# Performance work log

Hardware: AMD Instinct MI355X
Metric: run time of the kernel (lower is better)

Reference implementation:

```python
import jax, jax.numpy as jnp
import numpy as np

H, D_MODEL, LEN_Q, LEN_K, D_K, D_V = 16, 1024, 512, 2048, 64, 64
B = 4

def setup_inputs() -> dict:
    key = jax.random.key(0)
    ks = jax.random.split(key, 16)
    s = 0.02
    return {
        "Q": jax.random.normal(ks[0], (B, LEN_Q, D_MODEL), jnp.float32),
        "K": jax.random.normal(ks[1], (B, LEN_K, D_MODEL), jnp.float32),
        "V": jax.random.normal(ks[2], (B, LEN_K, D_MODEL), jnp.float32),
        "node_num": LEN_Q,
        "mask": jax.random.randint(ks[3], (B, LEN_K), 0, 2, jnp.int32),
        # params (stored as [in, out] so y = x @ W + b)
        "Wq": jax.random.normal(ks[4], (D_MODEL, H * D_K), jnp.float32) * s,
        "bq": jnp.zeros((H * D_K,), jnp.float32),
        "Wk": jax.random.normal(ks[5], (D_MODEL, H * D_K), jnp.float32) * s,
        "bk": jnp.zeros((H * D_K,), jnp.float32),
        "Wv": jax.random.normal(ks[6], (D_MODEL, H * D_V), jnp.float32) * s,
        "bv": jnp.zeros((H * D_V,), jnp.float32),
        "Wo": jax.random.normal(ks[7], (H * D_V, D_MODEL), jnp.float32) * s,
        "bo": jnp.zeros((D_MODEL,), jnp.float32),
        "gamma": jnp.ones((D_MODEL,), jnp.float32),
        "beta": jnp.zeros((D_MODEL,), jnp.float32),
    }

def _layernorm(x, gamma, beta, eps=1e-5):
    mu = jnp.mean(x, axis=-1, keepdims=True)
    var = jnp.mean((x - mu) ** 2, axis=-1, keepdims=True)
    return (x - mu) * jax.lax.rsqrt(var + eps) * gamma + beta

def reference(Q, K, V, node_num, mask, Wq, bq, Wk, bk, Wv, bv, Wo, bo, gamma, beta):
    b, lq, _ = Q.shape
    lk = K.shape[1]
    q = (Q @ Wq + bq).reshape(b, lq, H, D_K)   # [B, Lq, h, dk]
    k = (K @ Wk + bk).reshape(b, lk, H, D_K)   # [B, Lk, h, dk]
    v = (V @ Wv + bv).reshape(b, lk, H, D_V)   # [B, Lk, h, dv]
    scores = jnp.einsum('bqhd,bkhd->bhqk', q, k) / jnp.sqrt(jnp.float32(D_K))
    scores = jnp.where(mask[:, None, None, :] == 0, -jnp.inf, scores)
    alpha = jax.nn.softmax(scores, axis=-1)    # [B, h, Lq, Lk]
    out = jnp.einsum('bhqk,bkhd->bqhd', alpha, v).reshape(b, lq, H * D_V)
    out = out @ Wo + bo + Q                    # dropout is identity (eval)
    return _layernorm(out, gamma, beta)
```

## Files before the change

### kernel.cpp

```cpp
#include <hip/hip_runtime.h>

typedef __attribute__((ext_vector_type(8))) __bf16 bf16x8;
typedef __attribute__((ext_vector_type(4))) float f32x4;
typedef __attribute__((ext_vector_type(8))) unsigned short u16x8;

__device__ __forceinline__ float bf2f(unsigned short h) {
  union { unsigned int u; float f; } a; a.u = ((unsigned int)h) << 16; return a.f;
}
__device__ __forceinline__ unsigned short f2bf(float f) {
  union { float f; unsigned int u; } a; a.f = f;
  unsigned int u = a.u;
  u += 0x7fffu + ((u >> 16) & 1u);
  return (unsigned short)(u >> 16);
}
__device__ __forceinline__ float fast_exp2(float x) {
#if __has_builtin(__builtin_amdgcn_exp2f)
  return __builtin_amdgcn_exp2f(x);
#else
  return exp2f(x);
#endif
}
__device__ __forceinline__ bf16x8 ld_frag(const unsigned short* p) {
  bf16x8 r; __builtin_memcpy(&r, p, 16); return r;
}
__device__ __forceinline__ void cp16(unsigned short* dst, const unsigned short* src) {
  u16x8 t; __builtin_memcpy(&t, src, 16); __builtin_memcpy(dst, &t, 16);
}

#if __has_builtin(__builtin_amdgcn_global_load_lds)
typedef __attribute__((address_space(3))) unsigned int lds_u32;
typedef const __attribute__((address_space(1))) unsigned int glb_u32;
__device__ __forceinline__ void gload16(const unsigned short* g, unsigned short* l) {
  __builtin_amdgcn_global_load_lds((glb_u32*)g, (lds_u32*)l, 16, 0, 0);
}
#else
__device__ __forceinline__ void gload16(const unsigned short* g, unsigned short* l) {
  cp16(l, g);
}
#endif

__global__ __launch_bounds__(256) void cvt_kernel(
    const float* __restrict__ in, unsigned short* __restrict__ out, int n8)
{
  int i = blockIdx.x * 256 + threadIdx.x;
  if (i >= n8) return;
  float tf[8]; __builtin_memcpy(tf, &in[(size_t)i * 8], 32);
  unsigned short tu[8];
#pragma unroll
  for (int j = 0; j < 8; j++) tu[j] = f2bf(tf[j]);
  __builtin_memcpy(&out[(size_t)i * 8], tu, 16);
}

__global__ __launch_bounds__(256) void transpose4_kernel(
    const float* __restrict__ w0, const float* __restrict__ w1,
    const float* __restrict__ w2, const float* __restrict__ w3,
    unsigned short* __restrict__ out)
{
  __shared__ unsigned short tile[64 * 65];
  const int z = blockIdx.z;
  const float* in = (z == 0) ? w0 : (z == 1) ? w1 : (z == 2) ? w2 : w3;
  unsigned short* o = out + (size_t)z * 1048576;
  const int dim = 1024;
  const int t = threadIdx.x;
  const int n0 = blockIdx.x * 64, k0 = blockIdx.y * 64;
#pragma unroll
  for (int e = 0; e < 16; e++) {
    int idx = e * 256 + t;
    int i = idx >> 6, j = idx & 63;
    tile[i * 65 + j] = f2bf(in[(size_t)(k0 + i) * dim + n0 + j]);
  }
  __syncthreads();
#pragma unroll
  for (int e = 0; e < 16; e++) {
    int idx = e * 256 + t;
    int i = idx >> 6, j = idx & 63;
    o[(size_t)(n0 + i) * dim + k0 + j] = tile[j * 65 + i];
  }
}

__global__ __launch_bounds__(256) void gemm_bt_kernel(
    const unsigned short* __restrict__ A,
    const unsigned short* __restrict__ BT,
    const float* __restrict__ bias,
    unsigned short* __restrict__ C,
    int M, int N, int K, float cscale)
{
  __shared__ unsigned short As[128 * 32];
  __shared__ unsigned short Bs[128 * 32];
  const int tid  = threadIdx.x;
  const int wave = tid >> 6;
  const int lane = tid & 63;
  const int quad = lane >> 4;
  const int l16  = lane & 15;
  const int m0 = blockIdx.x * 128;
  const int n0 = blockIdx.y * 128;
  const int wm = (wave & 1) * 64;
  const int wn = (wave >> 1) * 64;

  const f32x4 fz = {0.0f, 0.0f, 0.0f, 0.0f};
  f32x4 acc[4][4];
#pragma unroll
  for (int i = 0; i < 4; i++)
#pragma unroll
    for (int j = 0; j < 4; j++) acc[i][j] = fz;

  const int srow0 = tid >> 2;
  const int scol  = (tid & 3) * 8;

  for (int k0 = 0; k0 < K; k0 += 32) {
#pragma unroll
    for (int i = 0; i < 2; i++) {
      int row = srow0 + i * 64;
      gload16(&A[(size_t)(m0 + row) * K + k0 + scol], &As[row * 32 + scol]);
      gload16(&BT[(size_t)(n0 + row) * K + k0 + scol], &Bs[row * 32 + scol]);
    }
    __syncthreads();
    bf16x8 afr[4], bfr[4];
#pragma unroll
    for (int mt = 0; mt < 4; mt++) afr[mt] = ld_frag(&As[(wm + mt * 16 + l16) * 32 + quad * 8]);
#pragma unroll
    for (int nt = 0; nt < 4; nt++) bfr[nt] = ld_frag(&Bs[(wn + nt * 16 + l16) * 32 + quad * 8]);
#pragma unroll
    for (int mt = 0; mt < 4; mt++)
#pragma unroll
      for (int nt = 0; nt < 4; nt++)
        acc[mt][nt] = __builtin_amdgcn_mfma_f32_16x16x32_bf16(afr[mt], bfr[nt], acc[mt][nt], 0, 0, 0);
    __syncthreads();
  }

#pragma unroll
  for (int nt = 0; nt < 4; nt++) {
    int col = n0 + wn + nt * 16 + l16;
    float bv = bias[col];
#pragma unroll
    for (int mt = 0; mt < 4; mt++) {
      int rowb = m0 + wm + mt * 16 + quad * 4;
#pragma unroll
      for (int r = 0; r < 4; r++)
        C[(size_t)(rowb + r) * N + col] = f2bf((acc[mt][nt][r] + bv) * cscale);
    }
  }
}

__global__ __launch_bounds__(256) void gemm_bt64_kernel(
    const unsigned short* __restrict__ A,
    const unsigned short* __restrict__ BT,
    const float* __restrict__ bias,
    unsigned short* __restrict__ C,
    int M, int N, int K, float cscale)
{
  __shared__ unsigned short As[64 * 32];
  __shared__ unsigned short Bs[128 * 32];
  const int tid  = threadIdx.x;
  const int wave = tid >> 6;
  const int lane = tid & 63;
  const int quad = lane >> 4;
  const int l16  = lane & 15;
  const int m0 = blockIdx.x * 64;
  const int n0 = blockIdx.y * 128;
  const int wm = (wave & 1) * 32;
  const int wn = (wave >> 1) * 64;

  const f32x4 fz = {0.0f, 0.0f, 0.0f, 0.0f};
  f32x4 acc[2][4];
#pragma unroll
  for (int i = 0; i < 2; i++)
#pragma unroll
    for (int j = 0; j < 4; j++) acc[i][j] = fz;

  const int srow0 = tid >> 2;
  const int scol  = (tid & 3) * 8;

  for (int k0 = 0; k0 < K; k0 += 32) {
    gload16(&A[(size_t)(m0 + srow0) * K + k0 + scol], &As[srow0 * 32 + scol]);
#pragma unroll
    for (int i = 0; i < 2; i++) {
      int row = srow0 + i * 64;
      gload16(&BT[(size_t)(n0 + row) * K + k0 + scol], &Bs[row * 32 + scol]);
    }
    __syncthreads();
    bf16x8 afr[2], bfr[4];
#pragma unroll
    for (int mt = 0; mt < 2; mt++) afr[mt] = ld_frag(&As[(wm + mt * 16 + l16) * 32 + quad * 8]);
#pragma unroll
    for (int nt = 0; nt < 4; nt++) bfr[nt] = ld_frag(&Bs[(wn + nt * 16 + l16) * 32 + quad * 8]);
#pragma unroll
    for (int mt = 0; mt < 2; mt++)
#pragma unroll
      for (int nt = 0; nt < 4; nt++)
        acc[mt][nt] = __builtin_amdgcn_mfma_f32_16x16x32_bf16(afr[mt], bfr[nt], acc[mt][nt], 0, 0, 0);
    __syncthreads();
  }

#pragma unroll
  for (int nt = 0; nt < 4; nt++) {
    int col = n0 + wn + nt * 16 + l16;
    float bv = bias[col];
#pragma unroll
    for (int mt = 0; mt < 2; mt++) {
      int rowb = m0 + wm + mt * 16 + quad * 4;
#pragma unroll
      for (int r = 0; r < 4; r++)
        C[(size_t)(rowb + r) * N + col] = f2bf((acc[mt][nt][r] + bv) * cscale);
    }
  }
}

__global__ __launch_bounds__(256) void gemm_vt_kernel(
    const unsigned short* __restrict__ A,
    const unsigned short* __restrict__ BT,
    const float* __restrict__ bias,
    unsigned short* __restrict__ vt)
{
  __shared__ unsigned short As[128 * 32];
  __shared__ unsigned short Bs[128 * 32];
  __shared__ unsigned short Ts[4][64 * 72];
  const int K = 1024;
  const int tid  = threadIdx.x;
  const int wave = tid >> 6;
  const int lane = tid & 63;
  const int quad = lane >> 4;
  const int l16  = lane & 15;
  const int m0 = blockIdx.x * 128;
  const int n0 = blockIdx.y * 128;
  const int wm = (wave & 1) * 64;
  const int wn = (wave >> 1) * 64;

  const f32x4 fz = {0.0f, 0.0f, 0.0f, 0.0f};
  f32x4 acc[4][4];
#pragma unroll
  for (int i = 0; i < 4; i++)
#pragma unroll
    for (int j = 0; j < 4; j++) acc[i][j] = fz;

  const int srow0 = tid >> 2;
  const int scol  = (tid & 3) * 8;

  for (int k0 = 0; k0 < K; k0 += 32) {
#pragma unroll
    for (int i = 0; i < 2; i++) {
      int row = srow0 + i * 64;
      gload16(&A[(size_t)(m0 + row) * K + k0 + scol], &As[row * 32 + scol]);
      gload16(&BT[(size_t)(n0 + row) * K + k0 + scol], &Bs[row * 32 + scol]);
    }
    __syncthreads();
    bf16x8 afr[4], bfr[4];
#pragma unroll
    for (int mt = 0; mt < 4; mt++) afr[mt] = ld_frag(&As[(wm + mt * 16 + l16) * 32 + quad * 8]);
#pragma unroll
    for (int nt = 0; nt < 4; nt++) bfr[nt] = ld_frag(&Bs[(wn + nt * 16 + l16) * 32 + quad * 8]);
#pragma unroll
    for (int mt = 0; mt < 4; mt++)
#pragma unroll
      for (int nt = 0; nt < 4; nt++)
        acc[mt][nt] = __builtin_amdgcn_mfma_f32_16x16x32_bf16(afr[mt], bfr[nt], acc[mt][nt], 0, 0, 0);
    __syncthreads();
  }

#pragma unroll
  for (int nt = 0; nt < 4; nt++) {
    float bv = bias[n0 + wn + nt * 16 + l16];
#pragma unroll
    for (int mt = 0; mt < 4; mt++)
#pragma unroll
      for (int r = 0; r < 4; r++)
        Ts[wave][(nt * 16 + l16) * 72 + mt * 16 + quad * 4 + r] = f2bf(acc[mt][nt][r] + bv);
  }
  {
    const int R0 = m0 + wm;
    const int b  = R0 >> 11;
    const int key0 = R0 & 2047;
    const int col = n0 + wn + lane;
    const int h  = col >> 6, dv = col & 63;
    const size_t vtrow = ((size_t)(b * 16 + h)) * 64 + dv;
#pragma unroll
    for (int jb = 0; jb < 8; jb++)
      cp16((unsigned short*)&vt[vtrow * 2048 + key0 + jb * 8],
           &Ts[wave][lane * 72 + jb * 8]);
  }
}

__device__ __forceinline__ void attn_load_tile(
    const unsigned short* __restrict__ kp, const unsigned short* __restrict__ vt,
    const int* __restrict__ mask, size_t kbase, size_t vbase, int mbase,
    int kt, int quad, int l16,
    bf16x8 (&bk)[4][2], bf16x8 (&bv)[4][2], int (&mk)[4])
{
#pragma unroll
  for (int nt = 0; nt < 4; nt++) {
    const size_t krow = kbase + ((size_t)(kt * 64 + nt * 16 + l16)) * 1024;
#pragma unroll
    for (int kc = 0; kc < 2; kc++)
      bk[nt][kc] = ld_frag(&kp[krow + kc * 32 + quad * 8]);
    mk[nt] = mask[mbase + kt * 64 + nt * 16 + l16];
  }
#pragma unroll
  for (int dvt = 0; dvt < 4; dvt++) {
    const size_t vrow = vbase + ((size_t)(dvt * 16 + l16)) * 2048 + kt * 64;
#pragma unroll
    for (int kc = 0; kc < 2; kc++)
      bv[dvt][kc] = ld_frag(&vt[vrow + kc * 32 + quad * 8]);
  }
}

__device__ __forceinline__ void attn_compute_tile(
    const bf16x8 (&aq)[2], const bf16x8 (&bk)[4][2], const bf16x8 (&bv)[4][2],
    const int (&mk)[4], unsigned short* Ps, int quad, int l16,
    float (&l_i)[4], f32x4 (&O)[4])
{
  const f32x4 fz = {0.0f, 0.0f, 0.0f, 0.0f};
  f32x4 s[4];
#pragma unroll
  for (int nt = 0; nt < 4; nt++) s[nt] = fz;
  __builtin_amdgcn_s_setprio(1);
#pragma unroll
  for (int nt = 0; nt < 4; nt++)
#pragma unroll
    for (int kc = 0; kc < 2; kc++)
      s[nt] = __builtin_amdgcn_mfma_f32_16x16x32_bf16(aq[kc], bk[nt][kc], s[nt], 0, 0, 0);
  __builtin_amdgcn_s_setprio(0);

#pragma unroll
  for (int nt = 0; nt < 4; nt++) {
    bool ok = (mk[nt] != 0);
#pragma unroll
    for (int r = 0; r < 4; r++) {
      float p = ok ? fast_exp2(s[nt][r]) : 0.0f;
      l_i[r] += p;
      Ps[(quad * 4 + r) * 72 + nt * 16 + l16] = f2bf(p);
    }
  }

  bf16x8 ap[2];
#pragma unroll
  for (int kc = 0; kc < 2; kc++)
    ap[kc] = ld_frag(&Ps[l16 * 72 + kc * 32 + quad * 8]);
  __builtin_amdgcn_s_setprio(1);
#pragma unroll
  for (int dvt = 0; dvt < 4; dvt++)
#pragma unroll
    for (int kc = 0; kc < 2; kc++)
      O[dvt] = __builtin_amdgcn_mfma_f32_16x16x32_bf16(ap[kc], bv[dvt][kc], O[dvt], 0, 0, 0);
  __builtin_amdgcn_s_setprio(0);
}

__global__ __launch_bounds__(256) void attn_kernel(
    const unsigned short* __restrict__ qp,
    const unsigned short* __restrict__ kp,
    const unsigned short* __restrict__ vt,
    const int* __restrict__ mask,
    unsigned short* __restrict__ attn)
{
  __shared__ unsigned short Ps[4][16 * 72];
  __shared__ unsigned short Opart[2][4][16 * 64];
  __shared__ float Lpart[2][4][16];

  const int tid  = threadIdx.x;
  const int wave = tid >> 6;
  const int lane = tid & 63;
  const int quad = lane >> 4;
  const int l16  = lane & 15;
  const int bid  = blockIdx.x;
  const int bh = bid & 63;
  const int qg = bid >> 6;
  const int b = bh >> 4, h = bh & 15;

  bf16x8 aq[2][2];
#pragma unroll
  for (int s = 0; s < 2; s++) {
    const size_t qbase = ((size_t)(b * 512 + qg * 32 + s * 16 + l16)) * 1024 + h * 64;
#pragma unroll
    for (int kc = 0; kc < 2; kc++)
      aq[s][kc] = ld_frag(&qp[qbase + kc * 32 + quad * 8]);
  }

  const f32x4 fz = {0.0f, 0.0f, 0.0f, 0.0f};
  float l_i[2][4];
  f32x4 O[2][4];
#pragma unroll
  for (int s = 0; s < 2; s++)
#pragma unroll
    for (int r = 0; r < 4; r++) { l_i[s][r] = 0.0f; O[s][r] = fz; }

  const size_t kbase = ((size_t)(b * 2048)) * 1024 + h * 64;
  const size_t vbase = ((size_t)(bh * 64)) * 2048;
  const int mbase = b * 2048;

  for (int it = 0; it < 8; it++) {
    const int kt = it * 4 + wave;
    bf16x8 bk[4][2], bv[4][2]; int mk[4];
    attn_load_tile(kp, vt, mask, kbase, vbase, mbase, kt, quad, l16, bk, bv, mk);
    attn_compute_tile(aq[0], bk, bv, mk, Ps[wave], quad, l16, l_i[0], O[0]);
    attn_compute_tile(aq[1], bk, bv, mk, Ps[wave], quad, l16, l_i[1], O[1]);
  }

#pragma unroll
  for (int s = 0; s < 2; s++)
#pragma unroll
    for (int off = 1; off < 16; off <<= 1)
#pragma unroll
      for (int r = 0; r < 4; r++) l_i[s][r] += __shfl_xor(l_i[s][r], off);

#pragma unroll
  for (int s = 0; s < 2; s++) {
#pragma unroll
    for (int dvt = 0; dvt < 4; dvt++)
#pragma unroll
      for (int r = 0; r < 4; r++)
        Opart[s][wave][(quad * 4 + r) * 64 + dvt * 16 + l16] = f2bf(O[s][dvt][r]);
    if (l16 == 0) {
#pragma unroll
      for (int r = 0; r < 4; r++)
        Lpart[s][wave][quad * 4 + r] = l_i[s][r];
    }
  }
  __syncthreads();

#pragma unroll
  for (int s = 0; s < 2; s++) {
#pragma unroll
    for (int r = 0; r < 4; r++) {
      const int row = quad * 4 + r;
      float lsum = Lpart[s][0][row] + Lpart[s][1][row] + Lpart[s][2][row] + Lpart[s][3][row];
      float inv = (lsum > 0.0f) ? (1.0f / lsum) : 0.0f;
      float of = 0.0f;
#pragma unroll
      for (int w = 0; w < 4; w++)
        of += bf2f(Opart[s][w][row * 64 + wave * 16 + l16]);
      const int grow = b * 512 + qg * 32 + s * 16 + row;
      attn[(size_t)grow * 1024 + h * 64 + wave * 16 + l16] = f2bf(of * inv);
    }
  }
}

__global__ __launch_bounds__(256) void ln_kernel(
    const unsigned short* __restrict__ x,
    const float* __restrict__ resid,
    const float* __restrict__ gamma,
    const float* __restrict__ beta,
    float* __restrict__ out)
{
  const int row = blockIdx.x;
  const int t = threadIdx.x;
  const int wave = t >> 6, lane = t & 63;
  __shared__ float red[8];
  float v[4];
  float s1 = 0.0f, s2 = 0.0f;
#pragma unroll
  for (int i = 0; i < 4; i++) {
    int e = t + i * 256;
    float val = bf2f(x[(size_t)row * 1024 + e]) + resid[(size_t)row * 1024 + e];
    v[i] = val; s1 += val; s2 += val * val;
  }
#pragma unroll
  for (int off = 1; off < 64; off <<= 1) { s1 += __shfl_xor(s1, off); s2 += __shfl_xor(s2, off); }
  if (lane == 0) { red[wave] = s1; red[4 + wave] = s2; }
  __syncthreads();
  s1 = red[0] + red[1] + red[2] + red[3];
  s2 = red[4] + red[5] + red[6] + red[7];
  float mu  = s1 * (1.0f / 1024.0f);
  float var = s2 * (1.0f / 1024.0f) - mu * mu;
  float rstd = rsqrtf(var + 1e-5f);
#pragma unroll
  for (int i = 0; i < 4; i++) {
    int e = t + i * 256;
    out[(size_t)row * 1024 + e] = (v[i] - mu) * rstd * gamma[e] + beta[e];
  }
}

extern "C" void kernel_launch(void* const* d_in, const int* in_sizes, int n_in,
                              void* d_out, int out_size, void* d_ws, size_t ws_size,
                              hipStream_t stream) {
  (void)out_size; (void)ws_size;
  const float* Q = (const float*)d_in[0];
  const float* K = (const float*)d_in[1];
  const float* V = (const float*)d_in[2];

  int ix = 3;
  if (ix < n_in && in_sizes[ix] == 1) ix++;
  const int* mask  = (const int*)d_in[ix++];
  const float* Wq = (const float*)d_in[ix++]; const float* bq = (const float*)d_in[ix++];
  const float* Wk = (const float*)d_in[ix++]; const float* bk = (const float*)d_in[ix++];
  const float* Wv = (const float*)d_in[ix++]; const float* bv = (const float*)d_in[ix++];
  const float* Wo = (const float*)d_in[ix++]; const float* bo = (const float*)d_in[ix++];
  const float* gm = (const float*)d_in[ix++]; const float* bt = (const float*)d_in[ix++];

  char* ws = (char*)d_ws;
  dim3 blk(256);

  unsigned short* WT4 = (unsigned short*)(ws);
  unsigned short* qp  = (unsigned short*)(ws + (8ull  << 20));
  unsigned short* kp  = (unsigned short*)(ws + (12ull << 20));
  unsigned short* vt  = (unsigned short*)(ws + (28ull << 20));
  unsigned short* at  = (unsigned short*)(ws + (44ull << 20));
  unsigned short* qb  = at;
  unsigned short* kvb = (unsigned short*)(ws + (48ull << 20));

  cvt_kernel<<<dim3(1024), blk, 0, stream>>>(Q, qb, 262144);
  cvt_kernel<<<dim3(4096), blk, 0, stream>>>(K, kvb, 1048576);
  transpose4_kernel<<<dim3(16, 16, 4), blk, 0, stream>>>(Wq, Wk, Wv, Wo, WT4);

  gemm_bt64_kernel<<<dim3(32, 8), blk, 0, stream>>>(qb, WT4, bq, qp, 2048, 1024, 1024, 0.18033688011112042f);
  gemm_bt_kernel<<<dim3(64, 8), blk, 0, stream>>>(kvb, WT4 + 1048576, bk, kp, 8192, 1024, 1024, 1.0f);
  cvt_kernel<<<dim3(4096), blk, 0, stream>>>(V, kvb, 1048576);
  gemm_vt_kernel<<<dim3(64, 8), blk, 0, stream>>>(kvb, WT4 + 2097152, bv, vt);

  attn_kernel<<<dim3(1024), blk, 0, stream>>>(qp, kp, vt, mask, at);

  gemm_bt64_kernel<<<dim3(32, 8), blk, 0, stream>>>(at, WT4 + 3145728, bo, qp, 2048, 1024, 1024, 1.0f);
  ln_kernel<<<dim3(2048), blk, 0, stream>>>(qp, Q, gm, bt, (float*)d_out);
}
```

Measured before the change: 317.8 us.

## Double-buffer GEMM LDS tiles and split attention blocks into 16-row query groups

All three projection GEMM kernels now use two LDS buffers. The next K-slice is issued before computing the current one, with explicit vmcnt waits and raw s_barrier calls in place of __syncthreads, so global loads overlap with MFMA work. The attention kernel now handles 16 query rows per block instead of 32 and launches twice as many blocks. This raises parallelism and cuts register and LDS use, but each K/V tile is loaded from memory twice as often. The hand-coded vmcnt counts assume gload16 is tracked by the vector-memory counter, so the prefetch is only correct if that holds.

Measured after the change: 366.9 us. 1.15x slower.

```diff
diff --git a/kernel.cpp b/kernel.cpp
--- a/kernel.cpp
+++ b/kernel.cpp
@@ -85,8 +85,8 @@
     unsigned short* __restrict__ C,
     int M, int N, int K, float cscale)
 {
-  __shared__ unsigned short As[128 * 32];
-  __shared__ unsigned short Bs[128 * 32];
+  __shared__ unsigned short As[2][128 * 32];
+  __shared__ unsigned short Bs[2][128 * 32];
   const int tid  = threadIdx.x;
   const int wave = tid >> 6;
   const int lane = tid & 63;
@@ -105,27 +105,38 @@
     for (int j = 0; j < 4; j++) acc[i][j] = fz;
 
   const int srow0 = tid >> 2;
+  const int srow1 = srow0 + 64;
   const int scol  = (tid & 3) * 8;
 
-  for (int k0 = 0; k0 < K; k0 += 32) {
-#pragma unroll
-    for (int i = 0; i < 2; i++) {
-      int row = srow0 + i * 64;
-      gload16(&A[(size_t)(m0 + row) * K + k0 + scol], &As[row * 32 + scol]);
-      gload16(&BT[(size_t)(n0 + row) * K + k0 + scol], &Bs[row * 32 + scol]);
+  auto stage = [&](int bf, int k0) {
+    gload16(&A[(size_t)(m0 + srow0) * K + k0 + scol], &As[bf][srow0 * 32 + scol]);
+    gload16(&A[(size_t)(m0 + srow1) * K + k0 + scol], &As[bf][srow1 * 32 + scol]);
+    gload16(&BT[(size_t)(n0 + srow0) * K + k0 + scol], &Bs[bf][srow0 * 32 + scol]);
+    gload16(&BT[(size_t)(n0 + srow1) * K + k0 + scol], &Bs[bf][srow1 * 32 + scol]);
+  };
+
+  const int NT = K >> 5;
+  stage(0, 0);
+  for (int kt = 0; kt < NT; ++kt) {
+    const int cur = kt & 1;
+    if (kt + 1 < NT) {
+      stage(cur ^ 1, (kt + 1) << 5);
+      asm volatile("s_waitcnt vmcnt(4)" ::: "memory");
+    } else {
+      asm volatile("s_waitcnt vmcnt(0)" ::: "memory");
     }
-    __syncthreads();
+    __builtin_amdgcn_s_barrier();
     bf16x8 afr[4], bfr[4];
 #pragma unroll
-    for (int mt = 0; mt < 4; mt++) afr[mt] = ld_frag(&As[(wm + mt * 16 + l16) * 32 + quad * 8]);
-#pragma unroll
-    for (int nt = 0; nt < 4; nt++) bfr[nt] = ld_frag(&Bs[(wn + nt * 16 + l16) * 32 + quad * 8]);
+    for (int mt = 0; mt < 4; mt++) afr[mt] = ld_frag(&As[cur][(wm + mt * 16 + l16) * 32 + quad * 8]);
+#pragma unroll
+    for (int nt = 0; nt < 4; nt++) bfr[nt] = ld_frag(&Bs[cur][(wn + nt * 16 + l16) * 32 + quad * 8]);
 #pragma unroll
     for (int mt = 0; mt < 4; mt++)
 #pragma unroll
       for (int nt = 0; nt < 4; nt++)
         acc[mt][nt] = __builtin_amdgcn_mfma_f32_16x16x32_bf16(afr[mt], bfr[nt], acc[mt][nt], 0, 0, 0);
-    __syncthreads();
+    __builtin_amdgcn_s_barrier();
   }
 
 #pragma unroll
@@ -149,8 +160,8 @@
     unsigned short* __restrict__ C,
     int M, int N, int K, float cscale)
 {
-  __shared__ unsigned short As[64 * 32];
-  __shared__ unsigned short Bs[128 * 32];
+  __shared__ unsigned short As[2][64 * 32];
+  __shared__ unsigned short Bs[2][128 * 32];
   const int tid  = threadIdx.x;
   const int wave = tid >> 6;
   const int lane = tid & 63;
@@ -169,27 +180,37 @@
     for (int j = 0; j < 4; j++) acc[i][j] = fz;
 
   const int srow0 = tid >> 2;
+  const int srow1 = srow0 + 64;
   const int scol  = (tid & 3) * 8;
 
-  for (int k0 = 0; k0 < K; k0 += 32) {
-    gload16(&A[(size_t)(m0 + srow0) * K + k0 + scol], &As[srow0 * 32 + scol]);
-#pragma unroll
-    for (int i = 0; i < 2; i++) {
-      int row = srow0 + i * 64;
-      gload16(&BT[(size_t)(n0 + row) * K + k0 + scol], &Bs[row * 32 + scol]);
+  auto stage = [&](int bf, int k0) {
+    gload16(&A[(size_t)(m0 + srow0) * K + k0 + scol], &As[bf][srow0 * 32 + scol]);
+    gload16(&BT[(size_t)(n0 + srow0) * K + k0 + scol], &Bs[bf][srow0 * 32 + scol]);
+    gload16(&BT[(size_t)(n0 + srow1) * K + k0 + scol], &Bs[bf][srow1 * 32 + scol]);
+  };
+
+  const int NT = K >> 5;
+  stage(0, 0);
+  for (int kt = 0; kt < NT; ++kt) {
+    const int cur = kt & 1;
+    if (kt + 1 < NT) {
+      stage(cur ^ 1, (kt + 1) << 5);
+      asm volatile("s_waitcnt vmcnt(3)" ::: "memory");
+    } else {
+      asm volatile("s_waitcnt vmcnt(0)" ::: "memory");
     }
-    __syncthreads();
+    __builtin_amdgcn_s_barrier();
     bf16x8 afr[2], bfr[4];
 #pragma unroll
-    for (int mt = 0; mt < 2; mt++) afr[mt] = ld_frag(&As[(wm + mt * 16 + l16) * 32 + quad * 8]);
-#pragma unroll
-    for (int nt = 0; nt < 4; nt++) bfr[nt] = ld_frag(&Bs[(wn + nt * 16 + l16) * 32 + quad * 8]);
+    for (int mt = 0; mt < 2; mt++) afr[mt] = ld_frag(&As[cur][(wm + mt * 16 + l16) * 32 + quad * 8]);
+#pragma unroll
+    for (int nt = 0; nt < 4; nt++) bfr[nt] = ld_frag(&Bs[cur][(wn + nt * 16 + l16) * 32 + quad * 8]);
 #pragma unroll
     for (int mt = 0; mt < 2; mt++)
 #pragma unroll
       for (int nt = 0; nt < 4; nt++)
         acc[mt][nt] = __builtin_amdgcn_mfma_f32_16x16x32_bf16(afr[mt], bfr[nt], acc[mt][nt], 0, 0, 0);
-    __syncthreads();
+    __builtin_amdgcn_s_barrier();
   }
 
 #pragma unroll
@@ -212,8 +233,8 @@
     const float* __restrict__ bias,
     unsigned short* __restrict__ vt)
 {
-  __shared__ unsigned short As[128 * 32];
-  __shared__ unsigned short Bs[128 * 32];
+  __shared__ unsigned short As[2][128 * 32];
+  __shared__ unsigned short Bs[2][128 * 32];
   __shared__ unsigned short Ts[4][64 * 72];
   const int K = 1024;
   const int tid  = threadIdx.x;
@@ -234,27 +255,38 @@
     for (int j = 0; j < 4; j++) acc[i][j] = fz;
 
   const int srow0 = tid >> 2;
+  const int srow1 = srow0 + 64;
   const int scol  = (tid & 3) * 8;
 
-  for (int k0 = 0; k0 < K; k0 += 32) {
-#pragma unroll
-    for (int i = 0; i < 2; i++) {
-      int row = srow0 + i * 64;
-      gload16(&A[(size_t)(m0 + row) * K + k0 + scol], &As[row * 32 + scol]);
-      gload16(&BT[(size_t)(n0 + row) * K + k0 + scol], &Bs[row * 32 + scol]);
+  auto stage = [&](int bf, int k0) {
+    gload16(&A[(size_t)(m0 + srow0) * K + k0 + scol], &As[bf][srow0 * 32 + scol]);
+    gload16(&A[(size_t)(m0 + srow1) * K + k0 + scol], &As[bf][srow1 * 32 + scol]);
+    gload16(&BT[(size_t)(n0 + srow0) * K + k0 + scol], &Bs[bf][srow0 * 32 + scol]);
+    gload16(&BT[(size_t)(n0 + srow1) * K + k0 + scol], &Bs[bf][srow1 * 32 + scol]);
+  };
+
+  const int NT = K >> 5;
+  stage(0, 0);
+  for (int kt = 0; kt < NT; ++kt) {
+    const int cur = kt & 1;
+    if (kt + 1 < NT) {
+      stage(cur ^ 1, (kt + 1) << 5);
+      asm volatile("s_waitcnt vmcnt(4)" ::: "memory");
+    } else {
+      asm volatile("s_waitcnt vmcnt(0)" ::: "memory");
     }
-    __syncthreads();
+    __builtin_amdgcn_s_barrier();
     bf16x8 afr[4], bfr[4];
 #pragma unroll
-    for (int mt = 0; mt < 4; mt++) afr[mt] = ld_frag(&As[(wm + mt * 16 + l16) * 32 + quad * 8]);
-#pragma unroll
-    for (int nt = 0; nt < 4; nt++) bfr[nt] = ld_frag(&Bs[(wn + nt * 16 + l16) * 32 + quad * 8]);
+    for (int mt = 0; mt < 4; mt++) afr[mt] = ld_frag(&As[cur][(wm + mt * 16 + l16) * 32 + quad * 8]);
+#pragma unroll
+    for (int nt = 0; nt < 4; nt++) bfr[nt] = ld_frag(&Bs[cur][(wn + nt * 16 + l16) * 32 + quad * 8]);
 #pragma unroll
     for (int mt = 0; mt < 4; mt++)
 #pragma unroll
       for (int nt = 0; nt < 4; nt++)
         acc[mt][nt] = __builtin_amdgcn_mfma_f32_16x16x32_bf16(afr[mt], bfr[nt], acc[mt][nt], 0, 0, 0);
-    __syncthreads();
+    __builtin_amdgcn_s_barrier();
   }
 
 #pragma unroll
@@ -352,8 +384,8 @@
     unsigned short* __restrict__ attn)
 {
   __shared__ unsigned short Ps[4][16 * 72];
-  __shared__ unsigned short Opart[2][4][16 * 64];
-  __shared__ float Lpart[2][4][16];
+  __shared__ unsigned short Opart[4][16 * 64];
+  __shared__ float Lpart[4][16];
 
   const int tid  = threadIdx.x;
   const int wave = tid >> 6;
@@ -365,22 +397,19 @@
   const int qg = bid >> 6;
   const int b = bh >> 4, h = bh & 15;
 
-  bf16x8 aq[2][2];
-#pragma unroll
-  for (int s = 0; s < 2; s++) {
-    const size_t qbase = ((size_t)(b * 512 + qg * 32 + s * 16 + l16)) * 1024 + h * 64;
+  bf16x8 aq[2];
+  {
+    const size_t qbase = ((size_t)(b * 512 + qg * 16 + l16)) * 1024 + h * 64;
 #pragma unroll
     for (int kc = 0; kc < 2; kc++)
-      aq[s][kc] = ld_frag(&qp[qbase + kc * 32 + quad * 8]);
+      aq[kc] = ld_frag(&qp[qbase + kc * 32 + quad * 8]);
   }
 
   const f32x4 fz = {0.0f, 0.0f, 0.0f, 0.0f};
-  float l_i[2][4];
-  f32x4 O[2][4];
-#pragma unroll
-  for (int s = 0; s < 2; s++)
-#pragma unroll
-    for (int r = 0; r < 4; r++) { l_i[s][r] = 0.0f; O[s][r] = fz; }
+  float l_i[4];
+  f32x4 O[4];
+#pragma unroll
+  for (int r = 0; r < 4; r++) { l_i[r] = 0.0f; O[r] = fz; }
 
   const size_t kbase = ((size_t)(b * 2048)) * 1024 + h * 64;
   const size_t vbase = ((size_t)(bh * 64)) * 2048;
@@ -390,46 +419,37 @@
     const int kt = it * 4 + wave;
     bf16x8 bk[4][2], bv[4][2]; int mk[4];
     attn_load_tile(kp, vt, mask, kbase, vbase, mbase, kt, quad, l16, bk, bv, mk);
-    attn_compute_tile(aq[0], bk, bv, mk, Ps[wave], quad, l16, l_i[0], O[0]);
-    attn_compute_tile(aq[1], bk, bv, mk, Ps[wave], quad, l16, l_i[1], O[1]);
-  }
-
-#pragma unroll
-  for (int s = 0; s < 2; s++)
-#pragma unroll
-    for (int off = 1; off < 16; off <<= 1)
-#pragma unroll
-      for (int r = 0; r < 4; r++) l_i[s][r] += __shfl_xor(l_i[s][r], off);
-
-#pragma unroll
-  for (int s = 0; s < 2; s++) {
-#pragma unroll
-    for (int dvt = 0; dvt < 4; dvt++)
-#pragma unroll
-      for (int r = 0; r < 4; r++)
-        Opart[s][wave][(quad * 4 + r) * 64 + dvt * 16 + l16] = f2bf(O[s][dvt][r]);
-    if (l16 == 0) {
-#pragma unroll
-      for (int r = 0; r < 4; r++)
-        Lpart[s][wave][quad * 4 + r] = l_i[s][r];
-    }
+    attn_compute_tile(aq, bk, bv, mk, Ps[wave], quad, l16, l_i, O);
+  }
+
+#pragma unroll
+  for (int off = 1; off < 16; off <<= 1)
+#pragma unroll
+    for (int r = 0; r < 4; r++) l_i[r] += __shfl_xor(l_i[r], off);
+
+#pragma unroll
+  for (int dvt = 0; dvt < 4; dvt++)
+#pragma unroll
+    for (int r = 0; r < 4; r++)
+      Opart[wave][(quad * 4 + r) * 64 + dvt * 16 + l16] = f2bf(O[dvt][r]);
+  if (l16 == 0) {
+#pragma unroll
+    for (int r = 0; r < 4; r++)
+      Lpart[wave][quad * 4 + r] = l_i[r];
   }
   __syncthreads();
 
 #pragma unroll
-  for (int s = 0; s < 2; s++) {
-#pragma unroll
-    for (int r = 0; r < 4; r++) {
-      const int row = quad * 4 + r;
-      float lsum = Lpart[s][0][row] + Lpart[s][1][row] + Lpart[s][2][row] + Lpart[s][3][row];
-      float inv = (lsum > 0.0f) ? (1.0f / lsum) : 0.0f;
-      float of = 0.0f;
-#pragma unroll
-      for (int w = 0; w < 4; w++)
-        of += bf2f(Opart[s][w][row * 64 + wave * 16 + l16]);
-      const int grow = b * 512 + qg * 32 + s * 16 + row;
-      attn[(size_t)grow * 1024 + h * 64 + wave * 16 + l16] = f2bf(of * inv);
-    }
+  for (int r = 0; r < 4; r++) {
+    const int row = quad * 4 + r;
+    float lsum = Lpart[0][row] + Lpart[1][row] + Lpart[2][row] + Lpart[3][row];
+    float inv = (lsum > 0.0f) ? (1.0f / lsum) : 0.0f;
+    float of = 0.0f;
+#pragma unroll
+    for (int w = 0; w < 4; w++)
+      of += bf2f(Opart[w][row * 64 + wave * 16 + l16]);
+    const int grow = b * 512 + qg * 16 + row;
+    attn[(size_t)grow * 1024 + h * 64 + wave * 16 + l16] = f2bf(of * inv);
   }
 }
 
@@ -505,7 +525,7 @@
   cvt_kernel<<<dim3(4096), blk, 0, stream>>>(V, kvb, 1048576);
   gemm_vt_kernel<<<dim3(64, 8), blk, 0, stream>>>(kvb, WT4 + 2097152, bv, vt);
 
-  attn_kernel<<<dim3(1024), blk, 0, stream>>>(qp, kp, vt, mask, at);
+  attn_kernel<<<dim3(2048), blk, 0, stream>>>(qp, kp, vt, mask, at);
 
   gemm_bt64_kernel<<<dim3(32, 8), blk, 0, stream>>>(at, WT4 + 3145728, bo, qp, 2048, 1024, 1024, 1.0f);
   ln_kernel<<<dim3(2048), blk, 0, stream>>>(qp, Q, gm, bt, (float*)d_out);
```
